# Kernel tuning notes

Hardware: AMD Instinct MI355X
Metric: run time of the kernel (lower is better)

Reference implementation:

```python
import jax, jax.numpy as jnp
import numpy as np

N, H, C = 50000, 256, 32  # nodes, hidden width of surrogate net, num_irreps channels
SIGN = 1.0


def setup_inputs() -> dict:
    key = jax.random.key(0)
    k0, k1, k2 = jax.random.split(key, 3)
    return {
        "pos": jax.random.normal(k0, (N, 3), dtype=jnp.float32),
        "W1": jax.random.normal(k1, (3, H), dtype=jnp.float32) / jnp.sqrt(3.0),
        "b1": jnp.zeros((H,), dtype=jnp.float32),
        "W2": jax.random.normal(k2, (H, C), dtype=jnp.float32) / jnp.sqrt(float(H)),
    }


def _net(pos, W1, b1, W2):
    # Surrogate upstream network producing data[of]: [N, C] features from [N, 3] positions.
    return jnp.tanh(pos @ W1 + b1) @ W2


def reference(pos, W1, b1, W2):
    # Torch loop: out[:, c, :] = d( sum_n of[n, c] ) / d pos  for each channel c.
    # Fused here: one vjp through the network, vmapped over the C one-hot channel cotangents.
    of, vjp_fn = jax.vjp(lambda p: _net(p, W1, b1, W2), pos)  # of: [N, C]
    eye = jnp.eye(of.shape[1], dtype=of.dtype)  # [C, C]

    def one_channel(e):
        # cotangent for channel c: ones in column c for every node (== grad of sum over nodes)
        return vjp_fn(jnp.broadcast_to(e[None, :], of.shape))[0]  # [N, 3]

    jac = jax.vmap(one_channel)(eye)  # [C, N, 3]
    return SIGN * jnp.transpose(jac, (1, 0, 2))  # [N, C, 3]
```

## Files before the change

kernel.cpp:

```cpp
#include <hip/hip_runtime.h>
#include <hip/hip_bf16.h>

#define N_NODES 50000
#define HDIM    256
#define CDIM    32
#define JDIM    96
#define NBLK    32
#define KSTEPS  8

typedef __attribute__((ext_vector_type(8))) short short8v;
typedef __attribute__((ext_vector_type(4))) float f32x4;

__device__ short  g_Bh[KSTEPS * 6 * 64 * 8];
__device__ short  g_Bl[KSTEPS * 6 * 64 * 8];
__device__ float4 g_Zc[HDIM];

template<bool ISBF>
__device__ __forceinline__ float ldv(const void* __restrict__ p, int i) {
    if constexpr (ISBF) return __bfloat162float(((const __hip_bfloat16*)p)[i]);
    else                return ((const float*)p)[i];
}

__device__ __forceinline__ bool detect_bf(const void* pos) {
    unsigned short uw = ((const unsigned short*)pos)[threadIdx.x & 63];
    int ef = (uw >> 7) & 0xFF;
    unsigned long long bal = __ballot(ef >= 100 && ef <= 140);
    return __popcll(bal) >= 56;
}

template<bool ISBF>
__device__ __forceinline__ void build_impl(const void* __restrict__ W1,
                                           const void* __restrict__ b1,
                                           const void* __restrict__ W2) {
    const int idx  = blockIdx.x * 256 + threadIdx.x;
    const int je   = idx & 7;
    const int lane = (idx >> 3) & 63;
    const int f    = idx >> 9;
    const int ks   = f / 6, jt = f % 6;
    const int h    = ks * 32 + (lane >> 4) * 8 + je;
    const int col  = jt * 16 + (lane & 15);
    float b = ldv<ISBF>(W1, (col % 3) * HDIM + h) * ldv<ISBF>(W2, h * CDIM + col / 3);
    __hip_bfloat16 hi = __float2bfloat16(b);
    float lo = b - __bfloat162float(hi);
    g_Bh[idx] = (short)__hip_bfloat16_raw(hi).x;
    g_Bl[idx] = (short)__hip_bfloat16_raw(__float2bfloat16(lo)).x;
    if (idx < HDIM) {
        g_Zc[idx] = make_float4(ldv<ISBF>(b1, idx),
                                ldv<ISBF>(W1, 0 * HDIM + idx),
                                ldv<ISBF>(W1, 1 * HDIM + idx),
                                ldv<ISBF>(W1, 2 * HDIM + idx));
    }
}

__global__ __launch_bounds__(256) void build_B(const void* __restrict__ pos,
                                               const void* __restrict__ W1,
                                               const void* __restrict__ b1,
                                               const void* __restrict__ W2) {
    if (detect_bf(pos)) build_impl<true >(W1, b1, W2);
    else                build_impl<false>(W1, b1, W2);
}

template<bool ISBF>
__device__ __forceinline__ void run_impl(
    const void* __restrict__ pos,
    void* __restrict__ out,
    short* __restrict__ SHL)
{
    const int tid  = threadIdx.x;
    const int lane = tid & 63;
    const int wv   = __builtin_amdgcn_readfirstlane(tid >> 6);

    {
        const int nl = tid & 31;
        const int hg = tid >> 5;
        const int n  = blockIdx.x * NBLK + nl;
        float p0 = 0.f, p1 = 0.f, p2 = 0.f;
        if (n < N_NODES) {
            p0 = ldv<ISBF>(pos, n * 3 + 0);
            p1 = ldv<ISBF>(pos, n * 3 + 1);
            p2 = ldv<ISBF>(pos, n * 3 + 2);
        }
        char* wb = (char*)SHL + nl * 512;
        const unsigned int swz = (unsigned)((nl & 7) << 4);
#pragma unroll 4
        for (int i = 0; i < 32; i += 4) {
            unsigned int hb[4], lb[4];
#pragma unroll
            for (int t = 0; t < 4; ++t) {
                const int h = hg * 32 + i + t;
                float4 zc = g_Zc[h];
                float z   = fmaf(p0, zc.y, fmaf(p1, zc.z, fmaf(p2, zc.w, zc.x)));
                float u   = __expf(-2.0f * fabsf(z));
                float inv = __builtin_amdgcn_rcpf(1.0f + u);
                float s   = 4.0f * u * inv * inv;
                hb[t] = __float_as_uint(s) & 0xffff0000u;
                lb[t] = __float_as_uint(s - __uint_as_float(hb[t]));
            }
            unsigned int ph0 = __builtin_amdgcn_perm(hb[1], hb[0], 0x07060302u);
            unsigned int ph1 = __builtin_amdgcn_perm(hb[3], hb[2], 0x07060302u);
            unsigned int pl0 = __builtin_amdgcn_perm(lb[1], lb[0], 0x07060302u);
            unsigned int pl1 = __builtin_amdgcn_perm(lb[3], lb[2], 0x07060302u);
            const unsigned int off = (unsigned)((hg * 64 + 2 * i)) ^ swz;
            *(uint2*)(wb + off)         = make_uint2(ph0, ph1);
            *(uint2*)(wb + 16384 + off) = make_uint2(pl0, pl1);
        }
    }
    __syncthreads();

    const int m0 = (wv >> 1) * 16;
    const int jh = wv & 1;
    const int arow = m0 + (lane & 15);
    const unsigned int sw   = (unsigned)((arow & 7) << 4);
    const unsigned int sw45 = sw & 0x30u;
    const unsigned int sw6  = sw & 0x40u;
    const char* base = (const char*)SHL + arow * 512
                     + (unsigned)(((lane >> 4) * 16) ^ sw45);
    const char* abE = base + sw6;
    const char* abO = base + (64 - sw6);

    const short8v* __restrict__ Bh = (const short8v*)g_Bh + jh * 192 + lane;
    const short8v* __restrict__ Bl = (const short8v*)g_Bl + jh * 192 + lane;

    f32x4 a0 = {}, a1 = {}, a2 = {};
#pragma unroll
    for (int ks = 0; ks < KSTEPS; ++ks) {
        const char* ap = ((ks & 1) ? abO : abE) + (ks & ~1) * 64;
        short8v ah = *(const short8v*)(ap);
        short8v al = *(const short8v*)(ap + 16384);
        short8v bh0 = Bh[ks * 384 +   0];
        short8v bh1 = Bh[ks * 384 +  64];
        short8v bh2 = Bh[ks * 384 + 128];
        short8v bl0 = Bl[ks * 384 +   0];
        short8v bl1 = Bl[ks * 384 +  64];
        short8v bl2 = Bl[ks * 384 + 128];
        a0 = __builtin_amdgcn_mfma_f32_16x16x32_bf16(ah, bh0, a0, 0, 0, 0);
        a1 = __builtin_amdgcn_mfma_f32_16x16x32_bf16(ah, bh1, a1, 0, 0, 0);
        a2 = __builtin_amdgcn_mfma_f32_16x16x32_bf16(ah, bh2, a2, 0, 0, 0);
        a0 = __builtin_amdgcn_mfma_f32_16x16x32_bf16(ah, bl0, a0, 0, 0, 0);
        a1 = __builtin_amdgcn_mfma_f32_16x16x32_bf16(ah, bl1, a1, 0, 0, 0);
        a2 = __builtin_amdgcn_mfma_f32_16x16x32_bf16(ah, bl2, a2, 0, 0, 0);
        a0 = __builtin_amdgcn_mfma_f32_16x16x32_bf16(al, bh0, a0, 0, 0, 0);
        a1 = __builtin_amdgcn_mfma_f32_16x16x32_bf16(al, bh1, a1, 0, 0, 0);
        a2 = __builtin_amdgcn_mfma_f32_16x16x32_bf16(al, bh2, a2, 0, 0, 0);
    }

    const int colb = jh * 48 + (lane & 15);
    const int rowb = blockIdx.x * NBLK + m0 + (lane >> 4) * 4;
    f32x4 accs[3] = {a0, a1, a2};
#pragma unroll
    for (int r = 0; r < 4; ++r) {
        const int n = rowb + r;
        if (n >= N_NODES) continue;
#pragma unroll
        for (int jt = 0; jt < 3; ++jt) {
            if constexpr (ISBF) {
                ((unsigned short*)out)[(size_t)n * JDIM + colb + jt * 16] =
                    __hip_bfloat16_raw(__float2bfloat16(accs[jt][r])).x;
            } else {
                ((float*)out)[(size_t)n * JDIM + colb + jt * 16] = accs[jt][r];
            }
        }
    }
}

__global__ __launch_bounds__(256, 5) void grad_fused(
    const void* __restrict__ pos,
    void* __restrict__ out)
{
    __shared__ short SHL[2 * NBLK * 256];

    if (detect_bf(pos)) run_impl<true >(pos, out, SHL);
    else                run_impl<false>(pos, out, SHL);
}

extern "C" void kernel_launch(void* const* d_in, const int* in_sizes, int n_in,
                              void* d_out, int out_size, void* d_ws, size_t ws_size,
                              hipStream_t stream) {
    (void)d_ws; (void)ws_size; (void)in_sizes; (void)n_in; (void)out_size;
    const void* pos = d_in[0];
    const void* W1  = d_in[1];
    const void* b1  = d_in[2];
    const void* W2  = d_in[3];

    build_B<<<(KSTEPS * 6 * 64 * 8) / 256, 256, 0, stream>>>(pos, W1, b1, W2);

    int grid = (N_NODES + NBLK - 1) / NBLK;
    grad_fused<<<grid, 256, 0, stream>>>(pos, d_out);
}
```

Before: 84.14 us.

## Switch to 32x32x16 MFMA with split-K across six waves and LDS reduction

Replaces the 16x16x32 MFMA tiling with 32x32x16 bf16 MFMA tiles. The block grows to 384 threads (6 waves), each handling one 32-column output tile over half of the hidden dimension. The two K-halves are combined through an LDS reduction before the store, and the B matrix is repacked into a single interleaved hi/lo buffer. This cuts MFMA instruction count and B loads per wave, at the cost of an extra barrier and LDS round trip plus a different occupancy target.

```diff
diff --git a/kernel.cpp b/kernel.cpp
--- a/kernel.cpp
+++ b/kernel.cpp
@@ -6,13 +6,12 @@
 #define CDIM    32
 #define JDIM    96
 #define NBLK    32
-#define KSTEPS  8
+#define NTHR    384
 
-typedef __attribute__((ext_vector_type(8))) short short8v;
-typedef __attribute__((ext_vector_type(4))) float f32x4;
+typedef __attribute__((ext_vector_type(8)))  short short8v;
+typedef __attribute__((ext_vector_type(16))) float f32x16;
 
-__device__ short  g_Bh[KSTEPS * 6 * 64 * 8];
-__device__ short  g_Bl[KSTEPS * 6 * 64 * 8];
+__device__ short  g_B[2 * 8 * 2 * 3 * 64 * 8];
 __device__ float4 g_Zc[HDIM];
 
 template<bool ISBF>
@@ -33,17 +32,20 @@
                                            const void* __restrict__ b1,
                                            const void* __restrict__ W2) {
     const int idx  = blockIdx.x * 256 + threadIdx.x;
-    const int je   = idx & 7;
+    const int e    = idx & 7;
     const int lane = (idx >> 3) & 63;
-    const int f    = idx >> 9;
-    const int ks   = f / 6, jt = f % 6;
-    const int h    = ks * 32 + (lane >> 4) * 8 + je;
-    const int col  = jt * 16 + (lane & 15);
+    int t = idx >> 9;
+    const int jt   = t % 3;  t /= 3;
+    const int hilo = t & 1;  t >>= 1;
+    const int ks   = t & 7;
+    const int kh   = t >> 3;
+    const int h    = kh * 128 + ks * 16 + ((lane >> 5) << 3) + e;
+    const int col  = jt * 32 + (lane & 31);
     float b = ldv<ISBF>(W1, (col % 3) * HDIM + h) * ldv<ISBF>(W2, h * CDIM + col / 3);
     __hip_bfloat16 hi = __float2bfloat16(b);
     float lo = b - __bfloat162float(hi);
-    g_Bh[idx] = (short)__hip_bfloat16_raw(hi).x;
-    g_Bl[idx] = (short)__hip_bfloat16_raw(__float2bfloat16(lo)).x;
+    g_B[idx] = hilo ? (short)__hip_bfloat16_raw(__float2bfloat16(lo)).x
+                    : (short)__hip_bfloat16_raw(hi).x;
     if (idx < HDIM) {
         g_Zc[idx] = make_float4(ldv<ISBF>(b1, idx),
                                 ldv<ISBF>(W1, 0 * HDIM + idx),
@@ -69,6 +71,8 @@
     const int tid  = threadIdx.x;
     const int lane = tid & 63;
     const int wv   = __builtin_amdgcn_readfirstlane(tid >> 6);
+    const int kh   = (wv >= 3) ? 1 : 0;
+    const int jt   = wv - 3 * kh;
 
     {
         const int nl = tid & 31;
@@ -82,12 +86,11 @@
         }
         char* wb = (char*)SHL + nl * 512;
         const unsigned int swz = (unsigned)((nl & 7) << 4);
-#pragma unroll 4
-        for (int i = 0; i < 32; i += 4) {
+        for (int c = hg; c < 64; c += 12) {
             unsigned int hb[4], lb[4];
 #pragma unroll
             for (int t = 0; t < 4; ++t) {
-                const int h = hg * 32 + i + t;
+                const int h = c * 4 + t;
                 float4 zc = g_Zc[h];
                 float z   = fmaf(p0, zc.y, fmaf(p1, zc.z, fmaf(p2, zc.w, zc.x)));
                 float u   = __expf(-2.0f * fabsf(z));
@@ -100,70 +103,70 @@
             unsigned int ph1 = __builtin_amdgcn_perm(hb[3], hb[2], 0x07060302u);
             unsigned int pl0 = __builtin_amdgcn_perm(lb[1], lb[0], 0x07060302u);
             unsigned int pl1 = __builtin_amdgcn_perm(lb[3], lb[2], 0x07060302u);
-            const unsigned int off = (unsigned)((hg * 64 + 2 * i)) ^ swz;
+            const unsigned int off = (unsigned)(8 * c) ^ swz;
             *(uint2*)(wb + off)         = make_uint2(ph0, ph1);
             *(uint2*)(wb + 16384 + off) = make_uint2(pl0, pl1);
         }
     }
     __syncthreads();
 
-    const int m0 = (wv >> 1) * 16;
-    const int jh = wv & 1;
-    const int arow = m0 + (lane & 15);
-    const unsigned int sw   = (unsigned)((arow & 7) << 4);
-    const unsigned int sw45 = sw & 0x30u;
-    const unsigned int sw6  = sw & 0x40u;
-    const char* base = (const char*)SHL + arow * 512
-                     + (unsigned)(((lane >> 4) * 16) ^ sw45);
-    const char* abE = base + sw6;
-    const char* abO = base + (64 - sw6);
+    const int arow = lane & 31;
+    const unsigned int sw = (unsigned)((arow & 7) << 4);
+    const char* base = (const char*)SHL + arow * 512 + kh * 256
+                     + (unsigned)(((lane >> 5) * 16) ^ (sw & 0x10u));
+    const char* pAs[4] = { base + ((0u * 32) ^ (sw & 0x60u)),
+                           base + ((1u * 32) ^ (sw & 0x60u)),
+                           base + ((2u * 32) ^ (sw & 0x60u)),
+                           base + ((3u * 32) ^ (sw & 0x60u)) };
+    const short8v* __restrict__ Bb =
+        (const short8v*)g_B + (kh * 48 + jt) * 64 + lane;
 
-    const short8v* __restrict__ Bh = (const short8v*)g_Bh + jh * 192 + lane;
-    const short8v* __restrict__ Bl = (const short8v*)g_Bl + jh * 192 + lane;
-
-    f32x4 a0 = {}, a1 = {}, a2 = {};
+    f32x16 acc = {};
 #pragma unroll
-    for (int ks = 0; ks < KSTEPS; ++ks) {
-        const char* ap = ((ks & 1) ? abO : abE) + (ks & ~1) * 64;
+    for (int ks = 0; ks < 8; ++ks) {
+        const char* ap = pAs[ks & 3] + (ks >> 2) * 128;
         short8v ah = *(const short8v*)(ap);
         short8v al = *(const short8v*)(ap + 16384);
-        short8v bh0 = Bh[ks * 384 +   0];
-        short8v bh1 = Bh[ks * 384 +  64];
-        short8v bh2 = Bh[ks * 384 + 128];
-        short8v bl0 = Bl[ks * 384 +   0];
-        short8v bl1 = Bl[ks * 384 +  64];
-        short8v bl2 = Bl[ks * 384 + 128];
-        a0 = __builtin_amdgcn_mfma_f32_16x16x32_bf16(ah, bh0, a0, 0, 0, 0);
-        a1 = __builtin_amdgcn_mfma_f32_16x16x32_bf16(ah, bh1, a1, 0, 0, 0);
-        a2 = __builtin_amdgcn_mfma_f32_16x16x32_bf16(ah, bh2, a2, 0, 0, 0);
-        a0 = __builtin_amdgcn_mfma_f32_16x16x32_bf16(ah, bl0, a0, 0, 0, 0);
-        a1 = __builtin_amdgcn_mfma_f32_16x16x32_bf16(ah, bl1, a1, 0, 0, 0);
-        a2 = __builtin_amdgcn_mfma_f32_16x16x32_bf16(ah, bl2, a2, 0, 0, 0);
-        a0 = __builtin_amdgcn_mfma_f32_16x16x32_bf16(al, bh0, a0, 0, 0, 0);
-        a1 = __builtin_amdgcn_mfma_f32_16x16x32_bf16(al, bh1, a1, 0, 0, 0);
-        a2 = __builtin_amdgcn_mfma_f32_16x16x32_bf16(al, bh2, a2, 0, 0, 0);
+        short8v bh = Bb[ks * 384];
+        short8v bl = Bb[ks * 384 + 192];
+        acc = __builtin_amdgcn_mfma_f32_32x32x16_bf16(ah, bh, acc, 0, 0, 0);
+        acc = __builtin_amdgcn_mfma_f32_32x32x16_bf16(ah, bl, acc, 0, 0, 0);
+        acc = __builtin_amdgcn_mfma_f32_32x32x16_bf16(al, bh, acc, 0, 0, 0);
     }
 
-    const int colb = jh * 48 + (lane & 15);
-    const int rowb = blockIdx.x * NBLK + m0 + (lane >> 4) * 4;
-    f32x4 accs[3] = {a0, a1, a2};
+    __syncthreads();
+    float* red = (float*)SHL;
+    if (kh == 1) {
+        float* rp = red + (jt * 64 + lane) * 18;
 #pragma unroll
-    for (int r = 0; r < 4; ++r) {
-        const int n = rowb + r;
-        if (n >= N_NODES) continue;
+        for (int r = 0; r < 16; r += 2)
+            *(float2*)(rp + r) = make_float2(acc[r], acc[r + 1]);
+    }
+    __syncthreads();
+    if (kh == 0) {
+        const float* rp = red + (jt * 64 + lane) * 18;
 #pragma unroll
-        for (int jt = 0; jt < 3; ++jt) {
+        for (int r = 0; r < 16; r += 2) {
+            float2 p = *(const float2*)(rp + r);
+            acc[r] += p.x; acc[r + 1] += p.y;
+        }
+        const int colb  = jt * 32 + (lane & 31);
+        const int rbase = blockIdx.x * NBLK + 4 * (lane >> 5);
+#pragma unroll
+        for (int r = 0; r < 16; ++r) {
+            const int n = rbase + (r & 3) + 8 * (r >> 2);
+            if (n >= N_NODES) continue;
             if constexpr (ISBF) {
-                ((unsigned short*)out)[(size_t)n * JDIM + colb + jt * 16] =
-                    __hip_bfloat16_raw(__float2bfloat16(accs[jt][r])).x;
+                ((unsigned short*)out)[(size_t)n * JDIM + colb] =
+                    __hip_bfloat16_raw(__float2bfloat16(acc[r])).x;
             } else {
-                ((float*)out)[(size_t)n * JDIM + colb + jt * 16] = accs[jt][r];
+                ((float*)out)[(size_t)n * JDIM + colb] = acc[r];
             }
         }
     }
 }
 
-__global__ __launch_bounds__(256, 5) void grad_fused(
+__global__ __launch_bounds__(NTHR, 7) void grad_fused(
     const void* __restrict__ pos,
     void* __restrict__ out)
 {
@@ -182,8 +185,8 @@
     const void* b1  = d_in[2];
     const void* W2  = d_in[3];
 
-    build_B<<<(KSTEPS * 6 * 64 * 8) / 256, 256, 0, stream>>>(pos, W1, b1, W2);
+    build_B<<<(2 * 8 * 2 * 3 * 64 * 8) / 256, 256, 0, stream>>>(pos, W1, b1, W2);
 
     int grid = (N_NODES + NBLK - 1) / NBLK;
-    grad_fused<<<grid, 256, 0, stream>>>(pos, d_out);
+    grad_fused<<<grid, NTHR, 0, stream>>>(pos, d_out);
 }
```

Measured after the change: 81.64 us. 3.0% less time.
